# Optimization experiments

Measured on AMD Instinct MI355X. Metric: run time of the kernel, lower is better.

Reference implementation:

```python
import jax, jax.numpy as jnp
import numpy as np

N_NODES = 100000
N_EDGES = 3200000
ALPHA = 0.1
ITERATIONS = 10


def setup_inputs() -> dict:
    key = jax.random.key(0)
    ks = jax.random.split(key, 7)
    features = jax.random.normal(ks[0], (N_NODES, 512), dtype=jnp.float32)
    W1 = jax.random.normal(ks[1], (512, 64), dtype=jnp.float32) * 0.05
    b1 = jax.random.normal(ks[2], (64,), dtype=jnp.float32) * 0.05
    W2 = jax.random.normal(ks[3], (64, 64), dtype=jnp.float32) * 0.05
    b2 = jax.random.normal(ks[4], (64,), dtype=jnp.float32) * 0.05
    edge_weights = jax.random.uniform(ks[5], (N_EDGES,), dtype=jnp.float32)
    edge_index = jax.random.randint(ks[6], (2, N_EDGES), 0, N_NODES, dtype=jnp.int64)
    return {"features": features, "W1": W1, "b1": b1, "W2": W2, "b2": b2,
            "edge_weights": edge_weights, "edge_index": edge_index}


def reference(features, W1, b1, W2, b2, edge_weights, edge_index):
    # dense MLP head (dropout disabled / eval mode)
    h = jax.nn.relu(features @ W1 + b1)          # [N, hidden]
    z = h @ W2 + b2                              # [N, labels]

    row, col = edge_index[0], edge_index[1]

    def step(p, _):
        # SpMM: out[row] += w * p[col]
        gathered = edge_weights[:, None] * p[col]                 # [E, labels]
        new = jax.ops.segment_sum(gathered, row, num_segments=N_NODES)
        p = (1.0 - ALPHA) * new + ALPHA * z
        return p, None

    p, _ = jax.lax.scan(step, z, None, length=ITERATIONS)
    return p
```

## Files before the change

kernel.cpp:

```cpp
#include <hip/hip_runtime.h>
#include <hip/hip_fp16.h>
#include <cmath>

#define N_NODES 100000
#define N_EDGES 3200000
#define ALPHA   0.1f
#define ITERS   10
#define NBUK    1024
#define RPB     98
#define CHUNK   8192
#define NCH     391

typedef __attribute__((ext_vector_type(8))) short short8;
typedef __attribute__((ext_vector_type(4))) float f32x4;

__device__ __forceinline__ short f2bf(float x) {
    union { float f; unsigned u; } v; v.f = x;
    unsigned r = v.u + 0x7fffu + ((v.u >> 16) & 1u);
    return (short)(r >> 16);
}

__global__ void prep_w(const float* __restrict__ W1, const float* __restrict__ W2,
                       short* __restrict__ W1t, short* __restrict__ W2t)
{
    int t = blockIdx.x * 256 + threadIdx.x;
    if (t < 512 * 64) { int k = t >> 6, c = t & 63; W1t[c * 512 + k] = f2bf(W1[t]); }
    if (t < 64 * 64)  { int k = t >> 6, c = t & 63; W2t[c * 64 + k]  = f2bf(W2[t]); }
}

__global__ __launch_bounds__(256) void mlp_mfma(
    const float* __restrict__ F, const short* __restrict__ W1t,
    const short* __restrict__ W2t, const float* __restrict__ b1,
    const float* __restrict__ b2, float* __restrict__ z, __half* __restrict__ q0)
{
    __shared__ short Ft[64 * 128];
    __shared__ short Wt[64 * 128];
    __shared__ short Ht[64 * 64];
    __shared__ short W2s[64 * 64];

    const int t  = threadIdx.x;
    const int l  = t & 63;
    const int wv = t >> 6;
    const int wr = wv * 16;
    const long base = (long)blockIdx.x * 64;

    const int sr = t >> 4;
    const int sk = (t & 15) * 8;

    float4 f0a, f0b, f1a, f1b, f2a, f2b, f3a, f3b;
    uint4  w0v, w1v, w2v, w3v;

#define LOAD_TILE(kt) do {                                                   \
    long g0 = base + sr;      if (g0 > N_NODES - 1) g0 = N_NODES - 1;        \
    long g1 = base + sr + 16; if (g1 > N_NODES - 1) g1 = N_NODES - 1;        \
    long g2 = base + sr + 32; if (g2 > N_NODES - 1) g2 = N_NODES - 1;        \
    long g3 = base + sr + 48; if (g3 > N_NODES - 1) g3 = N_NODES - 1;        \
    f0a = *(const float4*)(F + g0 * 512 + (kt) * 128 + sk);                  \
    f0b = *(const float4*)(F + g0 * 512 + (kt) * 128 + sk + 4);              \
    f1a = *(const float4*)(F + g1 * 512 + (kt) * 128 + sk);                  \
    f1b = *(const float4*)(F + g1 * 512 + (kt) * 128 + sk + 4);              \
    f2a = *(const float4*)(F + g2 * 512 + (kt) * 128 + sk);                  \
    f2b = *(const float4*)(F + g2 * 512 + (kt) * 128 + sk + 4);              \
    f3a = *(const float4*)(F + g3 * 512 + (kt) * 128 + sk);                  \
    f3b = *(const float4*)(F + g3 * 512 + (kt) * 128 + sk + 4);              \
    w0v = *(const uint4*)(W1t + (sr     ) * 512 + (kt) * 128 + sk);          \
    w1v = *(const uint4*)(W1t + (sr + 16) * 512 + (kt) * 128 + sk);          \
    w2v = *(const uint4*)(W1t + (sr + 32) * 512 + (kt) * 128 + sk);          \
    w3v = *(const uint4*)(W1t + (sr + 48) * 512 + (kt) * 128 + sk);          \
} while (0)

#define STORE_ROW(row, fa, fb, wreg) do {                                    \
    int r_ = (row);                                                          \
    short8 s_ = { f2bf((fa).x), f2bf((fa).y), f2bf((fa).z), f2bf((fa).w),    \
                  f2bf((fb).x), f2bf((fb).y), f2bf((fb).z), f2bf((fb).w) };  \
    *(short8*)&Ft[(r_ * 128 + sk) ^ ((r_ & 7) << 3)] = s_;                   \
    *(uint4*)&Wt[(r_ * 128 + sk) ^ ((r_ & 7) << 3)] = (wreg);                \
} while (0)

    LOAD_TILE(0);
    uint4 w2pa, w2pb;
    {
        int r2 = t >> 3, k2 = (t & 7) * 8;
        w2pa = *(const uint4*)(W2t + r2 * 64 + k2);
        w2pb = *(const uint4*)(W2t + (r2 + 32) * 64 + k2);
    }

    f32x4 acc[4] = {};
    for (int kt = 0; kt < 4; ++kt) {
        STORE_ROW(sr,      f0a, f0b, w0v);
        STORE_ROW(sr + 16, f1a, f1b, w1v);
        STORE_ROW(sr + 32, f2a, f2b, w2v);
        STORE_ROW(sr + 48, f3a, f3b, w3v);
        if (kt == 0) {
            int r2 = t >> 3, k2 = (t & 7) * 8;
            *(uint4*)&W2s[(r2 * 64 + k2) ^ ((r2 & 7) << 3)] = w2pa;
            *(uint4*)&W2s[((r2 + 32) * 64 + k2) ^ (((r2 + 32) & 7) << 3)] = w2pb;
        }
        __syncthreads();
        if (kt < 3) LOAD_TILE(kt + 1);
#pragma unroll
        for (int kc = 0; kc < 4; ++kc) {
            int kb = kc * 32 + (l >> 4) * 8;
            int ar = wr + (l & 15);
            short8 a = *(const short8*)&Ft[(ar * 128 + kb) ^ ((ar & 7) << 3)];
#pragma unroll
            for (int n = 0; n < 4; ++n) {
                int bc = n * 16 + (l & 15);
                short8 b = *(const short8*)&Wt[(bc * 128 + kb) ^ ((bc & 7) << 3)];
                acc[n] = __builtin_amdgcn_mfma_f32_16x16x32_bf16(a, b, acc[n], 0, 0, 0);
            }
        }
        __syncthreads();
    }

#pragma unroll
    for (int n = 0; n < 4; ++n) {
        int col = n * 16 + (l & 15);
        float bv = b1[col];
#pragma unroll
        for (int i = 0; i < 4; ++i) {
            int row = wr + (l >> 4) * 4 + i;
            float hv = fmaxf(acc[n][i] + bv, 0.0f);
            Ht[(row * 64 + col) ^ ((row & 7) << 3)] = f2bf(hv);
        }
    }
    f32x4 acc2[4] = {};
#pragma unroll
    for (int kc = 0; kc < 2; ++kc) {
        int kb = kc * 32 + (l >> 4) * 8;
        int ar = wr + (l & 15);
        short8 a = *(const short8*)&Ht[(ar * 64 + kb) ^ ((ar & 7) << 3)];
#pragma unroll
        for (int n = 0; n < 4; ++n) {
            int bc = n * 16 + (l & 15);
            short8 b = *(const short8*)&W2s[(bc * 64 + kb) ^ ((bc & 7) << 3)];
            acc2[n] = __builtin_amdgcn_mfma_f32_16x16x32_bf16(a, b, acc2[n], 0, 0, 0);
        }
    }
#pragma unroll
    for (int n = 0; n < 4; ++n) {
        int col = n * 16 + (l & 15);
        float bv = b2[col];
#pragma unroll
        for (int i = 0; i < 4; ++i) {
            long row = base + wr + (l >> 4) * 4 + i;
            if (row < N_NODES) {
                float zv = acc2[n][i] + bv;
                z[row * 64 + col]  = zv;
                q0[row * 64 + col] = __float2half(zv);
            }
        }
    }
#undef LOAD_TILE
#undef STORE_ROW
}

__global__ __launch_bounds__(256) void bhist(const int* __restrict__ rows, int* __restrict__ gh)
{
    __shared__ int cnt[NBUK];
    for (int i = threadIdx.x; i < NBUK; i += 256) cnt[i] = 0;
    __syncthreads();
    int base = blockIdx.x * CHUNK;
    int end  = base + CHUNK; if (end > N_EDGES) end = N_EDGES;
    for (int i = base + threadIdx.x; i < end; i += 256)
        atomicAdd(&cnt[rows[i] / RPB], 1);
    __syncthreads();
    for (int i = threadIdx.x; i < NBUK; i += 256)
        gh[i * NCH + blockIdx.x] = cnt[i];
}

__global__ __launch_bounds__(512) void bscan(int* __restrict__ gh, int* __restrict__ btot)
{
    __shared__ int s[512];
    int k = blockIdx.x;
    int t = threadIdx.x;
    int v = (t < NCH) ? gh[k * NCH + t] : 0;
    s[t] = v;
    __syncthreads();
    for (int off = 1; off < 512; off <<= 1) {
        int x = (t >= off) ? s[t - off] : 0;
        __syncthreads();
        s[t] += x;
        __syncthreads();
    }
    if (t < NCH) gh[k * NCH + t] = s[t] - v;
    if (t == NCH - 1) btot[k] = s[t];
}

__global__ __launch_bounds__(1024) void scan_btot(const int* __restrict__ btot, int* __restrict__ bbase)
{
    __shared__ int s[1024];
    int t = threadIdx.x;
    int v = btot[t];
    s[t] = v;
    __syncthreads();
    for (int off = 1; off < 1024; off <<= 1) {
        int x = (t >= off) ? s[t - off] : 0;
        __syncthreads();
        s[t] += x;
        __syncthreads();
    }
    bbase[t] = s[t] - v;
}

__global__ __launch_bounds__(256) void bpart(const int* __restrict__ rows, const int* __restrict__ cols,
                                             const float* __restrict__ w, const int* __restrict__ gh,
                                             const int* __restrict__ bbase, uint2* __restrict__ stg)
{
    __shared__ int cur[NBUK];
    int blk = blockIdx.x;
    for (int i = threadIdx.x; i < NBUK; i += 256)
        cur[i] = bbase[i] + gh[i * NCH + blk];
    __syncthreads();
    int base = blk * CHUNK;
    int end  = base + CHUNK; if (end > N_EDGES) end = N_EDGES;
    for (int i = base + threadIdx.x; i < end; i += 256) {
        int r = rows[i];
        int b = r / RPB;
        int pos = atomicAdd(&cur[b], 1);
        float ws = w[i] * ((1.0f - ALPHA) / 16.0f);
        unsigned meta = (unsigned)cols[i] | ((unsigned)(r - b * RPB) << 17);
        stg[pos] = make_uint2(meta, __float_as_uint(ws));
    }
}

__global__ __launch_bounds__(256) void bucket_sort2(const int* __restrict__ bbase,
                                                    const uint2* __restrict__ stg,
                                                    unsigned long long* __restrict__ cw,
                                                    int* __restrict__ rowp)
{
    __shared__ int ldeg[RPB];
    __shared__ int lcur[RPB];
    __shared__ int sc[128];
    const int b = blockIdx.x;
    const int rowlo = b * RPB;
    if (rowlo >= N_NODES) return;
    int rowhi = rowlo + RPB; if (rowhi > N_NODES) rowhi = N_NODES;
    const int nrows = rowhi - rowlo;
    const int t = threadIdx.x;
    const int base = bbase[b];
    const int cnt = ((b + 1 < NBUK) ? bbase[b + 1] : N_EDGES) - base;

    if (t < RPB) ldeg[t] = 0;
    __syncthreads();
    for (int j = t; j < cnt; j += 256)
        atomicAdd(&ldeg[stg[base + j].x >> 17], 1);
    __syncthreads();
    int v = 0;
    if (t < 128) { v = (t < nrows) ? ldeg[t] : 0; sc[t] = v; }
    __syncthreads();
    for (int off = 1; off < 128; off <<= 1) {
        int x = (t < 128 && t >= off) ? sc[t - off] : 0;
        __syncthreads();
        if (t < 128) sc[t] += x;
        __syncthreads();
    }
    if (t < nrows) {
        int rp = base + sc[t] - v;
        rowp[rowlo + t] = rp;
        lcur[t] = rp;
    }
    if (t == 0 && rowhi == N_NODES) rowp[N_NODES] = base + cnt;
    __syncthreads();
    for (int j = t; j < cnt; j += 256) {
        uint2 rec = stg[base + j];
        int roff = rec.x >> 17;
        unsigned col = rec.x & 0x1FFFFu;
        int pos = atomicAdd(&lcur[roff], 1);
        cw[pos] = (unsigned long long)col | ((unsigned long long)rec.y << 32);
    }
}

template <int LAST>
__global__ __launch_bounds__(256) void spmm_kernel(
    const int* __restrict__ rowp, const unsigned long long* __restrict__ cw,
    const __half* __restrict__ qin, const float* __restrict__ z,
    float beta, float outscale,
    __half* __restrict__ qout, float* __restrict__ out)
{
    const int wid = blockIdx.x * 4 + (threadIdx.x >> 6);
    if (wid >= N_NODES) return;
    const int lane = threadIdx.x & 63;
    const int sub  = lane >> 3;
    const int l8   = lane & 7;

    const int start = rowp[wid];
    const int end   = rowp[wid + 1];

    float a0 = 0, a1 = 0, a2 = 0, a3 = 0, a4 = 0, a5 = 0, a6 = 0, a7 = 0;
    int e = start + sub;
    for (; e + 8 < end; e += 16) {
        unsigned long long pc0 = cw[e];
        unsigned long long pc1 = cw[e + 8];
        int c0 = (int)(unsigned)pc0;
        int c1 = (int)(unsigned)pc1;
        float w0 = __uint_as_float((unsigned)(pc0 >> 32));
        float w1 = __uint_as_float((unsigned)(pc1 >> 32));
        uint4 v0 = *(const uint4*)(qin + (long)c0 * 64 + l8 * 8);
        uint4 v1 = *(const uint4*)(qin + (long)c1 * 64 + l8 * 8);
        float2 p;
        p = __half22float2(*(__half2*)&v0.x); a0 += w0 * p.x; a1 += w0 * p.y;
        p = __half22float2(*(__half2*)&v0.y); a2 += w0 * p.x; a3 += w0 * p.y;
        p = __half22float2(*(__half2*)&v0.z); a4 += w0 * p.x; a5 += w0 * p.y;
        p = __half22float2(*(__half2*)&v0.w); a6 += w0 * p.x; a7 += w0 * p.y;
        p = __half22float2(*(__half2*)&v1.x); a0 += w1 * p.x; a1 += w1 * p.y;
        p = __half22float2(*(__half2*)&v1.y); a2 += w1 * p.x; a3 += w1 * p.y;
        p = __half22float2(*(__half2*)&v1.z); a4 += w1 * p.x; a5 += w1 * p.y;
        p = __half22float2(*(__half2*)&v1.w); a6 += w1 * p.x; a7 += w1 * p.y;
    }
    if (e < end) {
        unsigned long long pc = cw[e];
        int c = (int)(unsigned)pc;
        float ww = __uint_as_float((unsigned)(pc >> 32));
        uint4 v0 = *(const uint4*)(qin + (long)c * 64 + l8 * 8);
        float2 p;
        p = __half22float2(*(__half2*)&v0.x); a0 += ww * p.x; a1 += ww * p.y;
        p = __half22float2(*(__half2*)&v0.y); a2 += ww * p.x; a3 += ww * p.y;
        p = __half22float2(*(__half2*)&v0.z); a4 += ww * p.x; a5 += ww * p.y;
        p = __half22float2(*(__half2*)&v0.w); a6 += ww * p.x; a7 += ww * p.y;
    }
    a0 += __shfl_xor(a0, 8);  a1 += __shfl_xor(a1, 8);
    a2 += __shfl_xor(a2, 8);  a3 += __shfl_xor(a3, 8);
    a4 += __shfl_xor(a4, 8);  a5 += __shfl_xor(a5, 8);
    a6 += __shfl_xor(a6, 8);  a7 += __shfl_xor(a7, 8);
    a0 += __shfl_xor(a0, 16); a1 += __shfl_xor(a1, 16);
    a2 += __shfl_xor(a2, 16); a3 += __shfl_xor(a3, 16);
    a4 += __shfl_xor(a4, 16); a5 += __shfl_xor(a5, 16);
    a6 += __shfl_xor(a6, 16); a7 += __shfl_xor(a7, 16);
    a0 += __shfl_xor(a0, 32); a1 += __shfl_xor(a1, 32);
    a2 += __shfl_xor(a2, 32); a3 += __shfl_xor(a3, 32);
    a4 += __shfl_xor(a4, 32); a5 += __shfl_xor(a5, 32);
    a6 += __shfl_xor(a6, 32); a7 += __shfl_xor(a7, 32);

    if (lane < 8) {
        float4 za = *(const float4*)(z + (long)wid * 64 + lane * 8);
        float4 zb = *(const float4*)(z + (long)wid * 64 + lane * 8 + 4);
        float o0 = a0 + beta * za.x, o1 = a1 + beta * za.y;
        float o2 = a2 + beta * za.z, o3 = a3 + beta * za.w;
        float o4 = a4 + beta * zb.x, o5 = a5 + beta * zb.y;
        float o6 = a6 + beta * zb.z, o7 = a7 + beta * zb.w;
        if (LAST) {
            float4 ra = { outscale * o0, outscale * o1, outscale * o2, outscale * o3 };
            float4 rb = { outscale * o4, outscale * o5, outscale * o6, outscale * o7 };
            *(float4*)(out + (long)wid * 64 + lane * 8)     = ra;
            *(float4*)(out + (long)wid * 64 + lane * 8 + 4) = rb;
        } else {
            __half2 h0 = __floats2half2_rn(o0, o1);
            __half2 h1 = __floats2half2_rn(o2, o3);
            __half2 h2 = __floats2half2_rn(o4, o5);
            __half2 h3 = __floats2half2_rn(o6, o7);
            uint4 pv = { *(unsigned*)&h0, *(unsigned*)&h1, *(unsigned*)&h2, *(unsigned*)&h3 };
            *(uint4*)(qout + (long)wid * 64 + lane * 8) = pv;
        }
    }
}

extern "C" void kernel_launch(void* const* d_in, const int* in_sizes, int n_in,
                              void* d_out, int out_size, void* d_ws, size_t ws_size,
                              hipStream_t stream)
{
    const float* features = (const float*)d_in[0];
    const float* W1 = (const float*)d_in[1];
    const float* b1 = (const float*)d_in[2];
    const float* W2 = (const float*)d_in[3];
    const float* b2 = (const float*)d_in[4];
    const float* ew = (const float*)d_in[5];
    const int*   ei = (const int*)d_in[6];
    const int* erow = ei;
    const int* ecol = ei + N_EDGES;
    float* out = (float*)d_out;

    char* ws = (char*)d_ws;
    size_t off = 0;
    auto alloc = [&](size_t bytes) {
        size_t c = off;
        off += (bytes + 255) & ~(size_t)255;
        return c;
    };
    float* z      = (float*)(ws + alloc((size_t)N_NODES * 64 * 4));
    __half* q0    = (__half*)(ws + alloc((size_t)N_NODES * 64 * 2));
    __half* qA    = (__half*)(ws + alloc((size_t)N_NODES * 64 * 2));
    unsigned long long* cw = (unsigned long long*)(ws + alloc((size_t)N_EDGES * 8));
    uint2* stg    = (uint2*)(ws + alloc((size_t)N_EDGES * 8));
    int*   gh     = (int*)  (ws + alloc((size_t)NBUK * NCH * 4));
    short* W1t    = (short*)(ws + alloc((size_t)512 * 64 * 2));
    short* W2t    = (short*)(ws + alloc((size_t)64 * 64 * 2));
    int*   rowp   = (int*)  (ws + alloc((size_t)(N_NODES + 1) * 4));
    int*   btot   = (int*)  (ws + alloc((size_t)NBUK * 4));
    int*   bbase  = (int*)  (ws + alloc((size_t)NBUK * 4));
    (void)ws_size; (void)in_sizes; (void)n_in; (void)out_size;

    prep_w<<<128, 256, 0, stream>>>(W1, W2, W1t, W2t);
    mlp_mfma<<<(N_NODES + 63) / 64, 256, 0, stream>>>(features, W1t, W2t, b1, b2, z, q0);

    bhist<<<NCH, 256, 0, stream>>>(erow, gh);
    bscan<<<NBUK, 512, 0, stream>>>(gh, btot);
    scan_btot<<<1, 1024, 0, stream>>>(btot, bbase);
    bpart<<<NCH, 256, 0, stream>>>(erow, ecol, ew, gh, bbase, stg);
    bucket_sort2<<<NBUK, 256, 0, stream>>>(bbase, stg, cw, rowp);

    const __half* qi = q0;
    for (int it = 1; it < ITERS; ++it) {
        __half* qo = (it & 1) ? qA : q0;
        float beta = (float)(0.1 / pow(16.0, (double)it));
        spmm_kernel<0><<<(N_NODES + 3) / 4, 256, 0, stream>>>(rowp, cw, qi, z, beta, 1.0f, qo, nullptr);
        qi = qo;
    }
    float beta10 = (float)(0.1 / pow(16.0, 10.0));
    float osc    = (float)pow(16.0, 10.0);
    spmm_kernel<1><<<(N_NODES + 3) / 4, 256, 0, stream>>>(rowp, cw, qi, z, beta10, osc, nullptr, out);
}
```

Baseline: 769.0 us.

## Store z in fp16 only, read MLP weights from global, stream edge records nontemporally

Drops the fp32 z buffer and keeps only the fp16 copy q0. The SpMM iterations read the half-precision z for the alpha term, and a third ping-pong buffer keeps q0 from being overwritten. The MLP kernel no longer stages W1/W2 through LDS and reads B fragments straight from global memory. CSR edge records are loaded with nontemporal hints, and the histogram/partition chunk size is doubled. These changes cut memory traffic and LDS use, at the cost of lower z precision and uncached global weight reads inside the MFMA loop.

```diff
diff --git a/kernel.cpp b/kernel.cpp
--- a/kernel.cpp
+++ b/kernel.cpp
@@ -8,8 +8,8 @@
 #define ITERS   10
 #define NBUK    1024
 #define RPB     98
-#define CHUNK   8192
-#define NCH     391
+#define CHUNK   16384
+#define NCH     196
 
 typedef __attribute__((ext_vector_type(8))) short short8;
 typedef __attribute__((ext_vector_type(4))) float f32x4;
@@ -31,12 +31,10 @@
 __global__ __launch_bounds__(256) void mlp_mfma(
     const float* __restrict__ F, const short* __restrict__ W1t,
     const short* __restrict__ W2t, const float* __restrict__ b1,
-    const float* __restrict__ b2, float* __restrict__ z, __half* __restrict__ q0)
+    const float* __restrict__ b2, __half* __restrict__ q0)
 {
     __shared__ short Ft[64 * 128];
-    __shared__ short Wt[64 * 128];
     __shared__ short Ht[64 * 64];
-    __shared__ short W2s[64 * 64];
 
     const int t  = threadIdx.x;
     const int l  = t & 63;
@@ -48,7 +46,6 @@
     const int sk = (t & 15) * 8;
 
     float4 f0a, f0b, f1a, f1b, f2a, f2b, f3a, f3b;
-    uint4  w0v, w1v, w2v, w3v;
 
 #define LOAD_TILE(kt) do {                                                   \
     long g0 = base + sr;      if (g0 > N_NODES - 1) g0 = N_NODES - 1;        \
@@ -63,39 +60,23 @@
     f2b = *(const float4*)(F + g2 * 512 + (kt) * 128 + sk + 4);              \
     f3a = *(const float4*)(F + g3 * 512 + (kt) * 128 + sk);                  \
     f3b = *(const float4*)(F + g3 * 512 + (kt) * 128 + sk + 4);              \
-    w0v = *(const uint4*)(W1t + (sr     ) * 512 + (kt) * 128 + sk);          \
-    w1v = *(const uint4*)(W1t + (sr + 16) * 512 + (kt) * 128 + sk);          \
-    w2v = *(const uint4*)(W1t + (sr + 32) * 512 + (kt) * 128 + sk);          \
-    w3v = *(const uint4*)(W1t + (sr + 48) * 512 + (kt) * 128 + sk);          \
 } while (0)
 
-#define STORE_ROW(row, fa, fb, wreg) do {                                    \
+#define STORE_ROW(row, fa, fb) do {                                          \
     int r_ = (row);                                                          \
     short8 s_ = { f2bf((fa).x), f2bf((fa).y), f2bf((fa).z), f2bf((fa).w),    \
                   f2bf((fb).x), f2bf((fb).y), f2bf((fb).z), f2bf((fb).w) };  \
     *(short8*)&Ft[(r_ * 128 + sk) ^ ((r_ & 7) << 3)] = s_;                   \
-    *(uint4*)&Wt[(r_ * 128 + sk) ^ ((r_ & 7) << 3)] = (wreg);                \
 } while (0)
 
     LOAD_TILE(0);
-    uint4 w2pa, w2pb;
-    {
-        int r2 = t >> 3, k2 = (t & 7) * 8;
-        w2pa = *(const uint4*)(W2t + r2 * 64 + k2);
-        w2pb = *(const uint4*)(W2t + (r2 + 32) * 64 + k2);
-    }
 
     f32x4 acc[4] = {};
     for (int kt = 0; kt < 4; ++kt) {
-        STORE_ROW(sr,      f0a, f0b, w0v);
-        STORE_ROW(sr + 16, f1a, f1b, w1v);
-        STORE_ROW(sr + 32, f2a, f2b, w2v);
-        STORE_ROW(sr + 48, f3a, f3b, w3v);
-        if (kt == 0) {
-            int r2 = t >> 3, k2 = (t & 7) * 8;
-            *(uint4*)&W2s[(r2 * 64 + k2) ^ ((r2 & 7) << 3)] = w2pa;
-            *(uint4*)&W2s[((r2 + 32) * 64 + k2) ^ (((r2 + 32) & 7) << 3)] = w2pb;
-        }
+        STORE_ROW(sr,      f0a, f0b);
+        STORE_ROW(sr + 16, f1a, f1b);
+        STORE_ROW(sr + 32, f2a, f2b);
+        STORE_ROW(sr + 48, f3a, f3b);
         __syncthreads();
         if (kt < 3) LOAD_TILE(kt + 1);
 #pragma unroll
@@ -106,7 +87,7 @@
 #pragma unroll
             for (int n = 0; n < 4; ++n) {
                 int bc = n * 16 + (l & 15);
-                short8 b = *(const short8*)&Wt[(bc * 128 + kb) ^ ((bc & 7) << 3)];
+                short8 b = *(const short8*)(W1t + bc * 512 + kt * 128 + kb);
                 acc[n] = __builtin_amdgcn_mfma_f32_16x16x32_bf16(a, b, acc[n], 0, 0, 0);
             }
         }
@@ -133,7 +114,7 @@
 #pragma unroll
         for (int n = 0; n < 4; ++n) {
             int bc = n * 16 + (l & 15);
-            short8 b = *(const short8*)&W2s[(bc * 64 + kb) ^ ((bc & 7) << 3)];
+            short8 b = *(const short8*)(W2t + bc * 64 + kb);
             acc2[n] = __builtin_amdgcn_mfma_f32_16x16x32_bf16(a, b, acc2[n], 0, 0, 0);
         }
     }
@@ -144,11 +125,8 @@
 #pragma unroll
         for (int i = 0; i < 4; ++i) {
             long row = base + wr + (l >> 4) * 4 + i;
-            if (row < N_NODES) {
-                float zv = acc2[n][i] + bv;
-                z[row * 64 + col]  = zv;
-                q0[row * 64 + col] = __float2half(zv);
-            }
+            if (row < N_NODES)
+                q0[row * 64 + col] = __float2half(acc2[n][i] + bv);
         }
     }
 #undef LOAD_TILE
@@ -274,7 +252,7 @@
 template <int LAST>
 __global__ __launch_bounds__(256) void spmm_kernel(
     const int* __restrict__ rowp, const unsigned long long* __restrict__ cw,
-    const __half* __restrict__ qin, const float* __restrict__ z,
+    const __half* __restrict__ qin, const __half* __restrict__ zh,
     float beta, float outscale,
     __half* __restrict__ qout, float* __restrict__ out)
 {
@@ -290,8 +268,8 @@
     float a0 = 0, a1 = 0, a2 = 0, a3 = 0, a4 = 0, a5 = 0, a6 = 0, a7 = 0;
     int e = start + sub;
     for (; e + 8 < end; e += 16) {
-        unsigned long long pc0 = cw[e];
-        unsigned long long pc1 = cw[e + 8];
+        unsigned long long pc0 = __builtin_nontemporal_load(&cw[e]);
+        unsigned long long pc1 = __builtin_nontemporal_load(&cw[e + 8]);
         int c0 = (int)(unsigned)pc0;
         int c1 = (int)(unsigned)pc1;
         float w0 = __uint_as_float((unsigned)(pc0 >> 32));
@@ -309,7 +287,7 @@
         p = __half22float2(*(__half2*)&v1.w); a6 += w1 * p.x; a7 += w1 * p.y;
     }
     if (e < end) {
-        unsigned long long pc = cw[e];
+        unsigned long long pc = __builtin_nontemporal_load(&cw[e]);
         int c = (int)(unsigned)pc;
         float ww = __uint_as_float((unsigned)(pc >> 32));
         uint4 v0 = *(const uint4*)(qin + (long)c * 64 + l8 * 8);
@@ -333,12 +311,15 @@
     a6 += __shfl_xor(a6, 32); a7 += __shfl_xor(a7, 32);
 
     if (lane < 8) {
-        float4 za = *(const float4*)(z + (long)wid * 64 + lane * 8);
-        float4 zb = *(const float4*)(z + (long)wid * 64 + lane * 8 + 4);
-        float o0 = a0 + beta * za.x, o1 = a1 + beta * za.y;
-        float o2 = a2 + beta * za.z, o3 = a3 + beta * za.w;
-        float o4 = a4 + beta * zb.x, o5 = a5 + beta * zb.y;
-        float o6 = a6 + beta * zb.z, o7 = a7 + beta * zb.w;
+        uint4 zv = *(const uint4*)(zh + (long)wid * 64 + lane * 8);
+        float2 z0 = __half22float2(*(__half2*)&zv.x);
+        float2 z1 = __half22float2(*(__half2*)&zv.y);
+        float2 z2 = __half22float2(*(__half2*)&zv.z);
+        float2 z3 = __half22float2(*(__half2*)&zv.w);
+        float o0 = a0 + beta * z0.x, o1 = a1 + beta * z0.y;
+        float o2 = a2 + beta * z1.x, o3 = a3 + beta * z1.y;
+        float o4 = a4 + beta * z2.x, o5 = a5 + beta * z2.y;
+        float o6 = a6 + beta * z3.x, o7 = a7 + beta * z3.y;
         if (LAST) {
             float4 ra = { outscale * o0, outscale * o1, outscale * o2, outscale * o3 };
             float4 rb = { outscale * o4, outscale * o5, outscale * o6, outscale * o7 };
@@ -377,9 +358,9 @@
         off += (bytes + 255) & ~(size_t)255;
         return c;
     };
-    float* z      = (float*)(ws + alloc((size_t)N_NODES * 64 * 4));
     __half* q0    = (__half*)(ws + alloc((size_t)N_NODES * 64 * 2));
     __half* qA    = (__half*)(ws + alloc((size_t)N_NODES * 64 * 2));
+    __half* qB    = (__half*)(ws + alloc((size_t)N_NODES * 64 * 2));
     unsigned long long* cw = (unsigned long long*)(ws + alloc((size_t)N_EDGES * 8));
     uint2* stg    = (uint2*)(ws + alloc((size_t)N_EDGES * 8));
     int*   gh     = (int*)  (ws + alloc((size_t)NBUK * NCH * 4));
@@ -391,7 +372,7 @@
     (void)ws_size; (void)in_sizes; (void)n_in; (void)out_size;
 
     prep_w<<<128, 256, 0, stream>>>(W1, W2, W1t, W2t);
-    mlp_mfma<<<(N_NODES + 63) / 64, 256, 0, stream>>>(features, W1t, W2t, b1, b2, z, q0);
+    mlp_mfma<<<(N_NODES + 63) / 64, 256, 0, stream>>>(features, W1t, W2t, b1, b2, q0);
 
     bhist<<<NCH, 256, 0, stream>>>(erow, gh);
     bscan<<<NBUK, 512, 0, stream>>>(gh, btot);
@@ -401,12 +382,12 @@
 
     const __half* qi = q0;
     for (int it = 1; it < ITERS; ++it) {
-        __half* qo = (it & 1) ? qA : q0;
+        __half* qo = (it & 1) ? qA : qB;
         float beta = (float)(0.1 / pow(16.0, (double)it));
-        spmm_kernel<0><<<(N_NODES + 3) / 4, 256, 0, stream>>>(rowp, cw, qi, z, beta, 1.0f, qo, nullptr);
+        spmm_kernel<0><<<(N_NODES + 3) / 4, 256, 0, stream>>>(rowp, cw, qi, q0, beta, 1.0f, qo, nullptr);
         qi = qo;
     }
     float beta10 = (float)(0.1 / pow(16.0, 10.0));
     float osc    = (float)pow(16.0, 10.0);
-    spmm_kernel<1><<<(N_NODES + 3) / 4, 256, 0, stream>>>(rowp, cw, qi, z, beta10, osc, nullptr, out);
-}
+    spmm_kernel<1><<<(N_NODES + 3) / 4, 256, 0, stream>>>(rowp, cw, qi, q0, beta10, osc, nullptr, out);
+}
```

Result: slower. 897.2 us (+16.7%).
